# Optimization experiments

Hardware: AMD Instinct MI355X
Metric: run time of the kernel (lower is better)

Reference implementation:

```python
import jax
import jax.numpy as jnp
from jax import lax
import numpy as np

Y_SIZE = 64
X_SIZE = 50000
T_LEN = 1_000_000


def setup_inputs() -> dict:
    key = jax.random.key(0)
    kx, kt, kb, kp = jax.random.split(key, 4)
    x = jax.random.randint(kx, (T_LEN,), 0, X_SIZE, dtype=jnp.int32)
    transition = jax.random.uniform(kt, (Y_SIZE, Y_SIZE), dtype=jnp.float32)
    transition = transition / jnp.sum(transition, axis=1, keepdims=True)
    b = jax.random.uniform(kb, (Y_SIZE, X_SIZE), dtype=jnp.float32)
    b = b / jnp.sum(b, axis=1, keepdims=True)
    pi = jax.random.uniform(kp, (Y_SIZE,), dtype=jnp.float32)
    pi = pi / jnp.sum(pi)
    return {"x": x, "transition": transition, "b": b, "pi": pi}


def reference(x, transition, b, pi):
    """HMM.alpha_scaling: scaled forward recurrence.

    alpha[0]   = normalize(b[:, x[0]] * pi)
    alpha[t]   = normalize((alpha[t-1] @ transition) * b[:, x[t]])
    Returns the full (T, y_size) matrix of normalized forward probabilities,
    matching the torch loop (every stored row ends up sum-normalized).
    """
    a0 = b[:, x[0]] * pi                      # (y,)
    a0 = a0 / jnp.sum(a0)
    emis = b[:, x[1:]].T                      # (T-1, y) gathered emission probs

    def step(carry, e):
        new = (carry @ transition) * e        # (y,)
        new = new / jnp.sum(new)              # per-step scaling
        return new, new

    _, rest = lax.scan(step, a0, emis)        # rest: (T-1, y)
    return jnp.concatenate([a0[None, :], rest], axis=0)  # (T, y)
```

## Files before the change

kernel.cpp:

```cpp
#include <hip/hip_runtime.h>

#define TLEN 1000000
#define YS 64
#define XS 50000
#define CHUNK 32
#define WARM 8
#define SPAN (CHUNK + WARM)
#define NWIN (CHUNK / 4)
#define NCHUNK (TLEN / CHUNK)
#define RPW 16
#define NW ((NCHUNK + RPW - 1) / RPW)
#define WPB 4
#define NBLK ((NW + WPB - 1) / WPB)
#define BSCALE ((float)XS)

typedef float f32x4 __attribute__((ext_vector_type(4)));
typedef short bf16x8 __attribute__((ext_vector_type(8)));
typedef unsigned int u32x4 __attribute__((ext_vector_type(4)));

__device__ __forceinline__ unsigned cvtpk(float lo, float hi) {
  unsigned r;
  asm("v_cvt_pk_bf16_f32 %0, %1, %2" : "=v"(r) : "v"(lo), "v"(hi));
  return r;
}
__device__ __forceinline__ unsigned short f2bf_rne(float f) {
  unsigned u = __float_as_uint(f);
  unsigned r = (u + 0x7FFFu + ((u >> 16) & 1u)) >> 16;
  return (unsigned short)r;
}
__device__ __forceinline__ float bfu_lo(unsigned d) { return __uint_as_float(d << 16); }
__device__ __forceinline__ float bfu_hi(unsigned d) { return __uint_as_float(d & 0xffff0000u); }
__device__ __forceinline__ int clamp01(int t) {
  t = t < 0 ? 0 : t;
  return t > (TLEN - 1) ? (TLEN - 1) : t;
}

union bfu { u32x4 u; bf16x8 b; };

template <bool USE_BT>
__global__ __launch_bounds__(256, 2) void hmm_fwd(
    const int* __restrict__ x, const float* __restrict__ A,
    const float* __restrict__ pi, const float* __restrict__ b,
    const unsigned* __restrict__ bpk, float* __restrict__ out)
{
  __shared__ __align__(16) float tile[WPB][64][64];
  const int wslot = threadIdx.x >> 6;
  const int wv = blockIdx.x * WPB + wslot;
  const int lane = threadIdx.x & 63;
  if (wv >= NW) return;
  const int g = lane >> 4, c15 = lane & 15;

  bf16x8 Af[4][2];
#pragma unroll
  for (int nt = 0; nt < 4; nt++) {
    int sout = 32 * (nt >> 1) + 8 * (c15 >> 2) + 4 * (nt & 1) + (c15 & 3);
#pragma unroll
    for (int h = 0; h < 2; h++) {
      bf16x8 v;
#pragma unroll
      for (int j = 0; j < 8; j++) {
        int sin = 32 * h + 8 * g + j;
        v[j] = (short)f2bf_rne(A[sin * YS + sout]);
      }
      Af[nt][h] = v;
    }
  }

  const int tj0 = (wv * RPW + c15) * CHUNK - WARM;
  const bool isw0 = (wv == 0);

  u32x4 cb0, cb1;
  { unsigned one2 = 0x3f803f80u; cb0 = (u32x4){one2, one2, one2, one2}; cb1 = cb0; }

  auto eload = [&](int xt, u32x4& L0, u32x4& L1) {
    if (USE_BT) {
      const u32x4* p = (const u32x4*)(bpk + (size_t)(unsigned)xt * 32);
      L0 = p[g];
      L1 = p[4 + g];
    } else {
      unsigned t0[4], t1[4];
#pragma unroll
      for (int d = 0; d < 4; d++) {
        int s = 8 * g + 2 * d;
        t0[d] = cvtpk(b[(size_t)s * XS + xt] * BSCALE,
                      b[(size_t)(s + 1) * XS + xt] * BSCALE);
        int s2 = 32 + 8 * g + 2 * d;
        t1[d] = cvtpk(b[(size_t)s2 * XS + xt] * BSCALE,
                      b[(size_t)(s2 + 1) * XS + xt] * BSCALE);
      }
      L0 = (u32x4){t0[0], t0[1], t0[2], t0[3]};
      L1 = (u32x4){t1[0], t1[1], t1[2], t1[3]};
    }
  };

  u32x4 e0L0, e0L1, e1L0, e1L1;
  eload(x[clamp01(tj0 + 0)], e0L0, e0L1);
  eload(x[clamp01(tj0 + 1)], e1L0, e1L1);
  int xr0 = x[clamp01(tj0 + 2)];
  int xr1 = x[clamp01(tj0 + 3)];

  const f32x4 z4 = {0.f, 0.f, 0.f, 0.f};

  auto stepf = [&](int sabs, u32x4& L0, u32x4& L1, int& xr) {
    bfu ub0, ub1; ub0.u = cb0; ub1.u = cb1;
    bf16x8 bb0 = ub0.b, bb1 = ub1.b;

    f32x4 D0 = __builtin_amdgcn_mfma_f32_16x16x32_bf16(Af[0][0], bb0, z4, 0, 0, 0);
    f32x4 D1 = __builtin_amdgcn_mfma_f32_16x16x32_bf16(Af[1][0], bb0, z4, 0, 0, 0);
    f32x4 D2 = __builtin_amdgcn_mfma_f32_16x16x32_bf16(Af[2][0], bb0, z4, 0, 0, 0);
    f32x4 D3 = __builtin_amdgcn_mfma_f32_16x16x32_bf16(Af[3][0], bb0, z4, 0, 0, 0);
    D0 = __builtin_amdgcn_mfma_f32_16x16x32_bf16(Af[0][1], bb1, D0, 0, 0, 0);
    D1 = __builtin_amdgcn_mfma_f32_16x16x32_bf16(Af[1][1], bb1, D1, 0, 0, 0);
    D2 = __builtin_amdgcn_mfma_f32_16x16x32_bf16(Af[2][1], bb1, D2, 0, 0, 0);
    D3 = __builtin_amdgcn_mfma_f32_16x16x32_bf16(Af[3][1], bb1, D3, 0, 0, 0);

    D0[0] *= bfu_lo(L0[0]); D0[1] *= bfu_hi(L0[0]); D0[2] *= bfu_lo(L0[1]); D0[3] *= bfu_hi(L0[1]);
    D1[0] *= bfu_lo(L0[2]); D1[1] *= bfu_hi(L0[2]); D1[2] *= bfu_lo(L0[3]); D1[3] *= bfu_hi(L0[3]);
    D2[0] *= bfu_lo(L1[0]); D2[1] *= bfu_hi(L1[0]); D2[2] *= bfu_lo(L1[1]); D2[3] *= bfu_hi(L1[1]);
    D3[0] *= bfu_lo(L1[2]); D3[1] *= bfu_hi(L1[2]); D3[2] *= bfu_lo(L1[3]); D3[3] *= bfu_hi(L1[3]);

    if (isw0 && sabs == WARM && c15 == 0) {
      int x0v = x[0];
#pragma unroll
      for (int nt = 0; nt < 4; nt++) {
#pragma unroll
        for (int j = 0; j < 4; j++) {
          int s = 32 * (nt >> 1) + 8 * g + 4 * (nt & 1) + j;
          float ov = pi[s] * b[(size_t)s * XS + x0v] * BSCALE;
          if (nt == 0) D0[j] = ov;
          else if (nt == 1) D1[j] = ov;
          else if (nt == 2) D2[j] = ov;
          else D3[j] = ov;
        }
      }
    }

    f32x4 vs = (D0 + D1) + (D2 + D3);
    float ssum = (vs.x + vs.y) + (vs.z + vs.w);
    ssum += __shfl_xor(ssum, 16);
    ssum += __shfl_xor(ssum, 32);
    float r0 = __builtin_amdgcn_rcpf(ssum);
    float rs = r0 * fmaf(-ssum, r0, 2.0f);
    f32x4 N0 = D0 * rs, N1 = D1 * rs, N2 = D2 * rs, N3 = D3 * rs;

    cb0 = (u32x4){cvtpk(N0[0], N0[1]), cvtpk(N0[2], N0[3]),
                  cvtpk(N1[0], N1[1]), cvtpk(N1[2], N1[3])};
    cb1 = (u32x4){cvtpk(N2[0], N2[1]), cvtpk(N2[2], N2[3]),
                  cvtpk(N3[0], N3[1]), cvtpk(N3[2], N3[3])};

    if (sabs >= WARM) {
      const int srel = (sabs - WARM) & 3;
      float* rowp = &tile[wslot][4 * c15 + srel][0];
      const int xk = (c15 & 7) << 2;
      *(f32x4*)&rowp[(8 * g)      ^ xk] = N0;
      *(f32x4*)&rowp[(8 * g + 4)  ^ xk] = N1;
      *(f32x4*)&rowp[(32 + 8 * g) ^ xk] = N2;
      *(f32x4*)&rowp[(36 + 8 * g) ^ xk] = N3;
    }

    eload(xr, L0, L1);
    xr = x[clamp01(tj0 + sabs + 4)];
  };

  for (int s = 0; s < WARM; s += 2) {
    stepf(s + 0, e0L0, e0L1, xr0);
    stepf(s + 1, e1L0, e1L1, xr1);
  }

  for (int w = 0; w < NWIN; w++) {
    const int sb = WARM + 4 * w;
    stepf(sb + 0, e0L0, e0L1, xr0);
    stepf(sb + 1, e1L0, e1L1, xr1);
    stepf(sb + 2, e0L0, e0L1, xr0);
    stepf(sb + 3, e1L0, e1L1, xr1);

    __builtin_amdgcn_sched_barrier(0);
    asm volatile("" ::: "memory");
#pragma unroll
    for (int c = 0; c < 16; c++) {
      int gc = wv * RPW + c;
      if (gc < NCHUNK) {
        f32x4 v = *(const f32x4*)&tile[wslot][4 * c + g][(c15 * 4) ^ ((c & 7) << 2)];
        __builtin_nontemporal_store(v,
            (f32x4*)(out + ((size_t)gc * CHUNK + 4 * w + g) * YS + c15 * 4));
      }
    }
    asm volatile("" ::: "memory");
    __builtin_amdgcn_sched_barrier(0);
  }
}

__global__ __launch_bounds__(256) void pack_b(
    const float* __restrict__ b, unsigned* __restrict__ bpk)
{
  __shared__ float tileb[64][65];
  int x0 = blockIdx.x << 6;
  int lane = threadIdx.x & 63;
  int w = threadIdx.x >> 6;
  int xg = x0 + lane;
#pragma unroll
  for (int yy = 0; yy < 64; yy += 4) {
    int y = yy + w;
    tileb[y][lane] = (xg < XS) ? b[(size_t)y * XS + xg] * BSCALE : 0.f;
  }
  __syncthreads();
  int d = threadIdx.x & 31;
  int xo = threadIdx.x >> 5;
#pragma unroll
  for (int pass = 0; pass < 8; pass++) {
    int xl = pass * 8 + xo;
    int xcur = x0 + xl;
    if (xcur < XS)
      bpk[(size_t)xcur * 32 + d] = cvtpk(tileb[2 * d][xl], tileb[2 * d + 1][xl]);
  }
}

extern "C" void kernel_launch(void* const* d_in, const int* in_sizes, int n_in,
                              void* d_out, int out_size, void* d_ws, size_t ws_size,
                              hipStream_t stream)
{
  const int*   x  = (const int*)d_in[0];
  const float* A  = (const float*)d_in[1];
  const float* b  = (const float*)d_in[2];
  const float* pi = (const float*)d_in[3];
  float* out = (float*)d_out;

  const size_t bpk_bytes = (size_t)XS * 32 * sizeof(unsigned);

  if (ws_size >= bpk_bytes) {
    unsigned* bpk = (unsigned*)d_ws;
    int tblocks = (XS + 63) / 64;
    pack_b<<<tblocks, 256, 0, stream>>>(b, bpk);
    hmm_fwd<true><<<NBLK, 256, 0, stream>>>(x, A, pi, b, bpk, out);
  } else {
    hmm_fwd<false><<<NBLK, 256, 0, stream>>>(x, A, pi, b, nullptr, out);
  }
}
```

Measured before the change: 75.92 us.

## Double chunk length and deepen emission prefetch to four buffered steps

Chunk length per lane grows, which cuts the share of redundant warmup steps and the number of waves. The emission prefetch ring goes from two to four slots, and x indices are read eight steps ahead to hide gather latency. The cost is a longer serial recurrence per wave, lower parallelism on the GPU, and more registers held for the prefetch buffers.

```diff
diff --git a/kernel.cpp b/kernel.cpp
--- a/kernel.cpp
+++ b/kernel.cpp
@@ -3,7 +3,7 @@
 #define TLEN 1000000
 #define YS 64
 #define XS 50000
-#define CHUNK 32
+#define CHUNK 64
 #define WARM 8
 #define SPAN (CHUNK + WARM)
 #define NWIN (CHUNK / 4)
@@ -93,15 +93,17 @@
     }
   };
 
-  u32x4 e0L0, e0L1, e1L0, e1L1;
-  eload(x[clamp01(tj0 + 0)], e0L0, e0L1);
-  eload(x[clamp01(tj0 + 1)], e1L0, e1L1);
-  int xr0 = x[clamp01(tj0 + 2)];
-  int xr1 = x[clamp01(tj0 + 3)];
+  u32x4 eL0[4], eL1[4];
+  int xv[4];
+#pragma unroll
+  for (int u = 0; u < 4; u++) {
+    eload(x[clamp01(tj0 + u)], eL0[u], eL1[u]);
+    xv[u] = x[clamp01(tj0 + 4 + u)];
+  }
 
   const f32x4 z4 = {0.f, 0.f, 0.f, 0.f};
 
-  auto stepf = [&](int sabs, u32x4& L0, u32x4& L1, int& xr) {
+  auto stepf = [&](int sabs, int u) {
     bfu ub0, ub1; ub0.u = cb0; ub1.u = cb1;
     bf16x8 bb0 = ub0.b, bb1 = ub1.b;
 
@@ -114,6 +116,7 @@
     D2 = __builtin_amdgcn_mfma_f32_16x16x32_bf16(Af[2][1], bb1, D2, 0, 0, 0);
     D3 = __builtin_amdgcn_mfma_f32_16x16x32_bf16(Af[3][1], bb1, D3, 0, 0, 0);
 
+    u32x4 L0 = eL0[u], L1 = eL1[u];
     D0[0] *= bfu_lo(L0[0]); D0[1] *= bfu_hi(L0[0]); D0[2] *= bfu_lo(L0[1]); D0[3] *= bfu_hi(L0[1]);
     D1[0] *= bfu_lo(L0[2]); D1[1] *= bfu_hi(L0[2]); D1[2] *= bfu_lo(L0[3]); D1[3] *= bfu_hi(L0[3]);
     D2[0] *= bfu_lo(L1[0]); D2[1] *= bfu_hi(L1[0]); D2[2] *= bfu_lo(L1[1]); D2[3] *= bfu_hi(L1[1]);
@@ -158,21 +161,23 @@
       *(f32x4*)&rowp[(36 + 8 * g) ^ xk] = N3;
     }
 
-    eload(xr, L0, L1);
-    xr = x[clamp01(tj0 + sabs + 4)];
+    eload(xv[u], eL0[u], eL1[u]);
+    xv[u] = x[clamp01(tj0 + sabs + 8)];
   };
 
-  for (int s = 0; s < WARM; s += 2) {
-    stepf(s + 0, e0L0, e0L1, xr0);
-    stepf(s + 1, e1L0, e1L1, xr1);
+  for (int s = 0; s < WARM; s += 4) {
+    stepf(s + 0, 0);
+    stepf(s + 1, 1);
+    stepf(s + 2, 2);
+    stepf(s + 3, 3);
   }
 
   for (int w = 0; w < NWIN; w++) {
     const int sb = WARM + 4 * w;
-    stepf(sb + 0, e0L0, e0L1, xr0);
-    stepf(sb + 1, e1L0, e1L1, xr1);
-    stepf(sb + 2, e0L0, e0L1, xr0);
-    stepf(sb + 3, e1L0, e1L1, xr1);
+    stepf(sb + 0, 0);
+    stepf(sb + 1, 1);
+    stepf(sb + 2, 2);
+    stepf(sb + 3, 3);
 
     __builtin_amdgcn_sched_barrier(0);
     asm volatile("" ::: "memory");
```

Measured after the change: 73.07 us. 1.04x faster.
